# Kernel tuning notes

Hardware: AMD Instinct MI355X
Metric: run time of the kernel (lower is better)

The kernel has to match this reference:

```python
import jax, jax.numpy as jnp
import numpy as np

N, E = 20000, 320000
MEM, IN, HID, H = 128, 256, 128, 2
C = HID               # per-head channels, uniform across layers (see shape constraints)
MSG, TD = 100, 100
ED = MSG + TD         # edge_dim = msg_dim + time_enc.out_channels
L = 3
LN_EPS = 1e-5


def setup_inputs() -> dict:
    key = jax.random.key(0)
    ks = jax.random.split(key, 20)
    f32 = jnp.float32

    def nrm(k, shape, fan):
        return jax.random.normal(k, shape, f32) * (1.0 / np.sqrt(fan)).astype(np.float32)

    return {
        "x": jax.random.normal(ks[0], (N, MEM), f32),
        "last_update": jax.random.uniform(ks[1], (N,), f32) * 1000.0,
        "edge_index": jax.random.randint(ks[2], (2, E), 0, N, jnp.int32),
        "t": jax.random.uniform(ks[3], (E,), f32) * 1000.0,
        "msg": jax.random.normal(ks[4], (E, MSG), f32),
        # TimeEncoder: cos(t * w + b), Linear(1, TD)
        "time_w": nrm(ks[5], (TD,), 1),
        "time_b": nrm(ks[6], (TD,), 1),
        # self.lin: memory_dim -> in_channels
        "lin_w": nrm(ks[7], (MEM, IN), MEM),
        "lin_b": jnp.zeros((IN,), f32),
        # stacked per-layer TransformerConv params (all layers are IN -> H*C = 256)
        "Wq": nrm(ks[8], (L, IN, H * C), IN),
        "bq": jnp.zeros((L, H * C), f32),
        "Wk": nrm(ks[9], (L, IN, H * C), IN),
        "bk": jnp.zeros((L, H * C), f32),
        "Wv": nrm(ks[10], (L, IN, H * C), IN),
        "bv": jnp.zeros((L, H * C), f32),
        "We": nrm(ks[11], (L, ED, H * C), ED),   # lin_edge, bias=False in PyG
        "Wsk": nrm(ks[12], (L, IN, H * C), IN),  # lin_skip (root weight)
        "bsk": jnp.zeros((L, H * C), f32),
        "ln_g": jnp.ones((L, IN), f32),
        "ln_b": jnp.zeros((L, IN), f32),
    }


def _layer_norm(x, g, b):
    mu = jnp.mean(x, axis=-1, keepdims=True)
    var = jnp.mean((x - mu) ** 2, axis=-1, keepdims=True)
    return (x - mu) * jax.lax.rsqrt(var + LN_EPS) * g + b


def _transformer_conv(h, src, dst, eattr, Wq, bq, Wk, bk, Wv, bv, We, Wsk, bsk):
    # h: [N, IN]; eattr: [E, ED]
    q = (h @ Wq + bq).reshape(N, H, C)
    k = (h @ Wk + bk).reshape(N, H, C)
    v = (h @ Wv + bv).reshape(N, H, C)
    e = (eattr @ We).reshape(E, H, C)          # projected edge features
    k_j = k[src] + e                           # [E, H, C]
    alpha = jnp.einsum('ehc,ehc->eh', q[dst], k_j) / np.float32(np.sqrt(C))
    # segment softmax over destination nodes (PyG softmax: exp(a - max)/ (sum + 1e-16))
    amax = jax.ops.segment_max(alpha, dst, num_segments=N)
    ea = jnp.exp(alpha - amax[dst])
    denom = jax.ops.segment_sum(ea, dst, num_segments=N)
    a = ea / (denom[dst] + 1e-16)              # [E, H]
    msg_out = (v[src] + e) * a[:, :, None]     # [E, H, C]
    agg = jax.ops.segment_sum(msg_out, dst, num_segments=N).reshape(N, H * C)
    return agg + h @ Wsk + bsk                 # root/skip connection


def reference(x, last_update, edge_index, t, msg,
              time_w, time_b, lin_w, lin_b,
              Wq, bq, Wk, bk, Wv, bv, We, Wsk, bsk, ln_g, ln_b):
    src, dst = edge_index[0], edge_index[1]
    rel_t = last_update[src] - t                       # [E]
    rel_t_enc = jnp.cos(rel_t[:, None] * time_w + time_b)  # TimeEncoder
    eattr = jnp.concatenate([rel_t_enc, msg], axis=-1)     # [E, ED]
    h = x @ lin_w + lin_b                              # memory_dim != in_channels
    for i in range(L):
        h_new = _transformer_conv(h, src, dst, eattr,
                                  Wq[i], bq[i], Wk[i], bk[i], Wv[i], bv[i],
                                  We[i], Wsk[i], bsk[i])
        h = _layer_norm(h + h_new, ln_g[i], ln_b[i])   # dropout is identity in eval
        if i < L - 1:
            h = jax.nn.silu(h)
    return h
```

## Files before the change

### kernel.cpp

```cpp
#include <hip/hip_runtime.h>
#include <math.h>

constexpr int N_NODES = 20000;
constexpr int N_EDGES = 320000;
constexpr int MEM_D   = 128;
constexpr int IN_D    = 256;
constexpr int HEADS   = 2;
constexpr int CH      = 128;
constexpr int MSG_D   = 100;
constexpr int TD_D    = 100;
constexpr int ED_D    = 200;
constexpr int LAYERS  = 3;

__global__ __launch_bounds__(256) void relt_kernel(
    const int* __restrict__ src, const float* __restrict__ last_update,
    const float* __restrict__ t, float* __restrict__ rel)
{
    int e = blockIdx.x * 256 + threadIdx.x;
    if (e < N_EDGES) rel[e] = last_update[src[e]] - t[e];
}

__global__ __launch_bounds__(256) void time_enc_kernel(
    const float* __restrict__ rel, const float* __restrict__ time_w,
    const float* __restrict__ time_b, float* __restrict__ ct)
{
    __shared__ float sw[TD_D], sb[TD_D];
    int tid = threadIdx.x;
    if (tid < TD_D) { sw[tid] = time_w[tid]; sb[tid] = time_b[tid]; }
    __syncthreads();
    const int total = N_EDGES * TD_D;
    for (int idx = blockIdx.x * 256 + tid; idx < total; idx += gridDim.x * 256) {
        int e = idx / TD_D;
        int d = idx - e * TD_D;
        ct[idx] = cosf(rel[e] * sw[d] + sb[d]);
    }
}

#define BM 64
#define BN 64
#define BK 16
__global__ __launch_bounds__(256) void gemm_f32_kernel(
    const float* __restrict__ A, int lda, long aoff,
    const float* __restrict__ B, int ldb, long boff,
    float* __restrict__ Cm, int ldc, long coff,
    const float* __restrict__ bias,
    int M, int Nn, int K, int accumulate)
{
    A  += (long)blockIdx.z * aoff;
    B  += (long)blockIdx.z * boff;
    Cm += (long)blockIdx.z * coff;

    __shared__ __align__(16) float As[BK][BM + 4];
    __shared__ __align__(16) float Bs[BK][BN + 4];
    int tid = threadIdx.x;
    int tx = tid & 15, ty = tid >> 4;
    int m0 = blockIdx.y * BM, n0 = blockIdx.x * BN;

    float acc[4][4];
#pragma unroll
    for (int i = 0; i < 4; ++i)
#pragma unroll
        for (int j = 0; j < 4; ++j) acc[i][j] = 0.f;

    for (int k0 = 0; k0 < K; k0 += BK) {
#pragma unroll
        for (int i = 0; i < 4; ++i) {
            int li = tid + i * 256;
            int mm = li >> 4, kk = li & 15;
            int gm = m0 + mm, gk = k0 + kk;
            float va = (gm < M && gk < K) ? A[(size_t)gm * lda + gk] : 0.f;
            As[kk][mm] = va;
        }
#pragma unroll
        for (int i = 0; i < 4; ++i) {
            int li = tid + i * 256;
            int kk = li >> 6, nn = li & 63;
            int gk = k0 + kk, gn = n0 + nn;
            float vb = (gk < K && gn < Nn) ? B[(size_t)gk * ldb + gn] : 0.f;
            Bs[kk][nn] = vb;
        }
        __syncthreads();
#pragma unroll
        for (int kk = 0; kk < BK; ++kk) {
            float4 a4 = *(const float4*)&As[kk][ty * 4];
            float4 b4 = *(const float4*)&Bs[kk][tx * 4];
            float av[4] = {a4.x, a4.y, a4.z, a4.w};
            float bv[4] = {b4.x, b4.y, b4.z, b4.w};
#pragma unroll
            for (int i = 0; i < 4; ++i)
#pragma unroll
                for (int j = 0; j < 4; ++j) acc[i][j] += av[i] * bv[j];
        }
        __syncthreads();
    }
#pragma unroll
    for (int i = 0; i < 4; ++i) {
        int gm = m0 + ty * 4 + i;
        if (gm >= M) continue;
#pragma unroll
        for (int j = 0; j < 4; ++j) {
            int gn = n0 + tx * 4 + j;
            if (gn >= Nn) continue;
            float r = acc[i][j];
            if (bias) r += bias[gn];
            size_t off = (size_t)gm * ldc + gn;
            if (accumulate) r += Cm[off];
            Cm[off] = r;
        }
    }
}

#define GBM 128
#define GBN 128
#define GBK 16
__global__ __launch_bounds__(256) void gemm4_f32_kernel(
    const float* __restrict__ A,
    const float* __restrict__ B0, const float* __restrict__ B1,
    const float* __restrict__ B2, const float* __restrict__ B3,
    float* __restrict__ C0, float* __restrict__ C1,
    float* __restrict__ C2, float* __restrict__ C3,
    const float* __restrict__ bias0, const float* __restrict__ bias1,
    const float* __restrict__ bias2, const float* __restrict__ bias3,
    int M)
{
    const float* B; float* C; const float* bias;
    switch (blockIdx.z) {
        case 0: B = B0; C = C0; bias = bias0; break;
        case 1: B = B1; C = C1; bias = bias1; break;
        case 2: B = B2; C = C2; bias = bias2; break;
        default: B = B3; C = C3; bias = bias3; break;
    }
    __shared__ __align__(16) float As[GBK][GBM + 4];
    __shared__ __align__(16) float Bs[GBK][GBN + 4];
    int tid = threadIdx.x;
    int tx = tid & 15, ty = tid >> 4;
    int m0 = blockIdx.y * GBM, n0 = blockIdx.x * GBN;

    float acc00[4][4], acc01[4][4], acc10[4][4], acc11[4][4];
#pragma unroll
    for (int i = 0; i < 4; ++i)
#pragma unroll
        for (int j = 0; j < 4; ++j) {
            acc00[i][j] = 0.f; acc01[i][j] = 0.f;
            acc10[i][j] = 0.f; acc11[i][j] = 0.f;
        }

    for (int k0 = 0; k0 < IN_D; k0 += GBK) {
#pragma unroll
        for (int i = 0; i < 2; ++i) {
            int f = tid + i * 256;
            int row = f >> 2, cb = (f & 3) * 4;
            int gm = m0 + row;
            float4 v;
            if (gm < M) v = *(const float4*)(A + (size_t)gm * IN_D + k0 + cb);
            else { v.x = v.y = v.z = v.w = 0.f; }
            As[cb + 0][row] = v.x;
            As[cb + 1][row] = v.y;
            As[cb + 2][row] = v.z;
            As[cb + 3][row] = v.w;
        }
#pragma unroll
        for (int i = 0; i < 2; ++i) {
            int f = tid + i * 256;
            int kr = f >> 5, cb = (f & 31) * 4;
            float4 v = *(const float4*)(B + (size_t)(k0 + kr) * IN_D + n0 + cb);
            *(float4*)&Bs[kr][cb] = v;
        }
        __syncthreads();
#pragma unroll
        for (int kk = 0; kk < GBK; ++kk) {
            float4 A0 = *(const float4*)&As[kk][ty * 4];
            float4 A1 = *(const float4*)&As[kk][64 + ty * 4];
            float4 Bv0 = *(const float4*)&Bs[kk][tx * 4];
            float4 Bv1 = *(const float4*)&Bs[kk][64 + tx * 4];
            float a0[4] = {A0.x, A0.y, A0.z, A0.w};
            float a1[4] = {A1.x, A1.y, A1.z, A1.w};
            float b0[4] = {Bv0.x, Bv0.y, Bv0.z, Bv0.w};
            float b1[4] = {Bv1.x, Bv1.y, Bv1.z, Bv1.w};
#pragma unroll
            for (int i = 0; i < 4; ++i)
#pragma unroll
                for (int j = 0; j < 4; ++j) {
                    acc00[i][j] += a0[i] * b0[j];
                    acc01[i][j] += a0[i] * b1[j];
                    acc10[i][j] += a1[i] * b0[j];
                    acc11[i][j] += a1[i] * b1[j];
                }
        }
        __syncthreads();
    }
#pragma unroll
    for (int hm = 0; hm < 2; ++hm) {
#pragma unroll
        for (int i = 0; i < 4; ++i) {
            int gm = m0 + hm * 64 + ty * 4 + i;
            if (gm >= M) continue;
            int gn0 = n0 + tx * 4;
            int gn1 = n0 + 64 + tx * 4;
            float4 r0, r1;
            if (hm == 0) {
                r0.x = acc00[i][0]; r0.y = acc00[i][1]; r0.z = acc00[i][2]; r0.w = acc00[i][3];
                r1.x = acc01[i][0]; r1.y = acc01[i][1]; r1.z = acc01[i][2]; r1.w = acc01[i][3];
            } else {
                r0.x = acc10[i][0]; r0.y = acc10[i][1]; r0.z = acc10[i][2]; r0.w = acc10[i][3];
                r1.x = acc11[i][0]; r1.y = acc11[i][1]; r1.z = acc11[i][2]; r1.w = acc11[i][3];
            }
            r0.x += bias[gn0 + 0]; r0.y += bias[gn0 + 1];
            r0.z += bias[gn0 + 2]; r0.w += bias[gn0 + 3];
            r1.x += bias[gn1 + 0]; r1.y += bias[gn1 + 1];
            r1.z += bias[gn1 + 2]; r1.w += bias[gn1 + 3];
            *(float4*)(C + (size_t)gm * IN_D + gn0) = r0;
            *(float4*)(C + (size_t)gm * IN_D + gn1) = r1;
        }
    }
}

__global__ __launch_bounds__(256) void transpose_we_kernel(
    const float* __restrict__ We_l, float* __restrict__ WeT)
{
    int idx = blockIdx.x * 256 + threadIdx.x;
    if (idx >= HEADS * CH * ED_D) return;
    int hh = idx / (CH * ED_D);
    int r = idx - hh * (CH * ED_D);
    int c = r / ED_D;
    int d = r - c * ED_D;
    WeT[idx] = We_l[(size_t)d * IN_D + hh * CH + c];
}

__global__ __launch_bounds__(256) void hist_kernel(const int* __restrict__ dst,
                                                   int* __restrict__ counts)
{
    int e = blockIdx.x * 256 + threadIdx.x;
    if (e < N_EDGES) atomicAdd(&counts[dst[e]], 1);
}

__global__ __launch_bounds__(1024) void scan_kernel(const int* __restrict__ counts,
                                                    int* __restrict__ offsets)
{
    __shared__ int buf[1024];
    __shared__ int carry;
    int tid = threadIdx.x;
    if (tid == 0) carry = 0;
    __syncthreads();
    for (int base = 0; base < N_NODES; base += 1024) {
        int v = (base + tid < N_NODES) ? counts[base + tid] : 0;
        buf[tid] = v;
        __syncthreads();
        for (int off = 1; off < 1024; off <<= 1) {
            int tmp = (tid >= off) ? buf[tid - off] : 0;
            __syncthreads();
            buf[tid] += tmp;
            __syncthreads();
        }
        int incl = buf[tid];
        if (base + tid < N_NODES) offsets[base + tid] = carry + incl - v;
        int blocktot = buf[1023];
        __syncthreads();
        if (tid == 0) carry += blocktot;
        __syncthreads();
    }
    if (tid == 0) offsets[N_NODES] = carry;
}

__global__ __launch_bounds__(256) void copy_int_kernel(const int* __restrict__ a,
                                                       int* __restrict__ b, int n)
{
    int i = blockIdx.x * 256 + threadIdx.x;
    if (i < n) b[i] = a[i];
}

__global__ __launch_bounds__(256) void scatter_kernel(const int* __restrict__ dst,
                                                      int* __restrict__ cursor,
                                                      int* __restrict__ perm)
{
    int e = blockIdx.x * 256 + threadIdx.x;
    if (e < N_EDGES) {
        int p = atomicAdd(&cursor[dst[e]], 1);
        perm[p] = e;
    }
}

__global__ __launch_bounds__(256) void fused_attn_kernel(
    const int* __restrict__ perm, const int* __restrict__ offsets,
    const int* __restrict__ src,
    const float* __restrict__ qmat, const float* __restrict__ kmat,
    const float* __restrict__ vmat, const float* __restrict__ qWe,
    const float* __restrict__ ct, const float* __restrict__ msg,
    float* __restrict__ agg, float* __restrict__ wea)
{
    int n = blockIdx.x;
    int tid = threadIdx.x;
    int start = offsets[n], end = offsets[n + 1];

    __shared__ __align__(16) float sq[IN_D];
    __shared__ float sqw[HEADS * ED_D];
    __shared__ float salpha[64][2];
    __shared__ int   ssrc[64], sedge[64];
    __shared__ float red[256];
    __shared__ float s_m[2], s_s[2], s_r[2];

    sq[tid] = qmat[(size_t)n * IN_D + tid];
    for (int i = tid; i < HEADS * ED_D; i += 256)
        sqw[i] = qWe[(size_t)n * (HEADS * ED_D) + i];
    if (tid < 2) { s_m[tid] = -INFINITY; s_s[tid] = 0.f; }
    __syncthreads();

    float acc = 0.f;
    float wacc_a = 0.f, wacc_b = 0.f;
    const int head_c = tid >> 7;
    const int ha = (tid < ED_D) ? 0 : 1;
    const int da = (tid < ED_D) ? tid : tid - ED_D;
    const int idx2 = tid + 256;
    const int db = idx2 - ED_D;
    const int grp = tid >> 7, lid = tid & 127;
    const int wv = tid >> 6, lane = tid & 63, head = lane >> 5, l = lane & 31;

    for (int base = start; base < end; base += 64) {
        int cnt = min(64, end - base);
        if (tid < cnt) {
            int e = perm[base + tid];
            sedge[tid] = e;
            ssrc[tid] = src[e];
        }
        __syncthreads();

        for (int j = wv; j < cnt; j += 4) {
            int e = sedge[j], s = ssrc[j];
            float4 ka = *(const float4*)(kmat + (size_t)s * IN_D + head * CH + l * 4);
            float4 qa = *(const float4*)(&sq[head * CH + l * 4]);
            float sum = qa.x * ka.x + qa.y * ka.y + qa.z * ka.z + qa.w * ka.w;
            const float* ctrow = ct + (size_t)e * TD_D;
            const float* msgrow = msg + (size_t)e * MSG_D;
            const float* qw = &sqw[head * ED_D];
#pragma unroll
            for (int it = 0; it < 7; ++it) {
                int dd = l + it * 32;
                if (dd < ED_D) {
                    float ev = (dd < TD_D) ? ctrow[dd] : msgrow[dd - TD_D];
                    sum += qw[dd] * ev;
                }
            }
#pragma unroll
            for (int off = 16; off > 0; off >>= 1) sum += __shfl_xor(sum, off, 64);
            if (l == 0) salpha[j][head] = sum * 0.08838834764831845f;
        }
        __syncthreads();

        float pm = -INFINITY;
        for (int j = lid; j < cnt; j += 128) pm = fmaxf(pm, salpha[j][grp]);
        red[tid] = pm;
        __syncthreads();
        for (int s2 = 64; s2 > 0; s2 >>= 1) {
            if (lid < s2) red[tid] = fmaxf(red[tid], red[tid + s2]);
            __syncthreads();
        }
        if (lid == 0) {
            float cm = red[tid];
            float mold = s_m[grp];
            float mnew = fmaxf(mold, cm);
            s_r[grp] = expf(mold - mnew);
            s_m[grp] = mnew;
            s_s[grp] *= s_r[grp];
        }
        __syncthreads();

        float psum = 0.f;
        for (int j = lid; j < cnt; j += 128) {
            float p = expf(salpha[j][grp] - s_m[grp]);
            salpha[j][grp] = p;
            psum += p;
        }
        red[tid] = psum;
        __syncthreads();
        for (int s2 = 64; s2 > 0; s2 >>= 1) {
            if (lid < s2) red[tid] += red[tid + s2];
            __syncthreads();
        }
        if (lid == 0) s_s[grp] += red[tid];

        acc *= s_r[head_c];
        wacc_a *= s_r[ha];
        wacc_b *= s_r[1];
        for (int tt = 0; tt < cnt; ++tt) {
            float p_c = salpha[tt][head_c];
            acc += p_c * vmat[(size_t)ssrc[tt] * IN_D + tid];
            int e = sedge[tt];
            float ev_a = (da < TD_D) ? ct[(size_t)e * TD_D + da]
                                     : msg[(size_t)e * MSG_D + (da - TD_D)];
            wacc_a += salpha[tt][ha] * ev_a;
            if (idx2 < HEADS * ED_D) {
                float ev_b = (db < TD_D) ? ct[(size_t)e * TD_D + db]
                                         : msg[(size_t)e * MSG_D + (db - TD_D)];
                wacc_b += salpha[tt][1] * ev_b;
            }
        }
        __syncthreads();
    }

    float inv_c = 1.f / (s_s[head_c] + 1e-16f);
    agg[(size_t)n * IN_D + tid] = acc * inv_c;
    float inv_a = 1.f / (s_s[ha] + 1e-16f);
    wea[(size_t)n * (HEADS * ED_D) + tid] = wacc_a * inv_a;
    if (idx2 < HEADS * ED_D) {
        float inv_b = 1.f / (s_s[1] + 1e-16f);
        wea[(size_t)n * (HEADS * ED_D) + idx2] = wacc_b * inv_b;
    }
}

__global__ __launch_bounds__(256) void ln_kernel(
    const float* __restrict__ hprev, const float* __restrict__ agg,
    const float* __restrict__ hskip,
    const float* __restrict__ g, const float* __restrict__ b,
    float* __restrict__ out, int do_silu)
{
    int n = blockIdx.x, c = threadIdx.x;
    size_t off = (size_t)n * IN_D + c;
    float y = hprev[off] + agg[off] + hskip[off];
    __shared__ float red[256];
    red[c] = y;
    __syncthreads();
    for (int s = 128; s > 0; s >>= 1) {
        if (c < s) red[c] += red[c + s];
        __syncthreads();
    }
    float mu = red[0] * (1.f / 256.f);
    __syncthreads();
    float dy = y - mu;
    red[c] = dy * dy;
    __syncthreads();
    for (int s = 128; s > 0; s >>= 1) {
        if (c < s) red[c] += red[c + s];
        __syncthreads();
    }
    float var = red[0] * (1.f / 256.f);
    float r = dy * (1.f / sqrtf(var + 1e-5f)) * g[c] + b[c];
    if (do_silu) r = r / (1.f + expf(-r));
    out[off] = r;
}

extern "C" void kernel_launch(void* const* d_in, const int* in_sizes, int n_in,
                              void* d_out, int out_size, void* d_ws, size_t ws_size,
                              hipStream_t stream)
{
    const float* x           = (const float*)d_in[0];
    const float* last_update = (const float*)d_in[1];
    const int*   edge_index  = (const int*)d_in[2];
    const float* t           = (const float*)d_in[3];
    const float* msg         = (const float*)d_in[4];
    const float* time_w      = (const float*)d_in[5];
    const float* time_b      = (const float*)d_in[6];
    const float* lin_w       = (const float*)d_in[7];
    const float* lin_b       = (const float*)d_in[8];
    const float* Wq          = (const float*)d_in[9];
    const float* bq          = (const float*)d_in[10];
    const float* Wk          = (const float*)d_in[11];
    const float* bk          = (const float*)d_in[12];
    const float* Wv          = (const float*)d_in[13];
    const float* bv          = (const float*)d_in[14];
    const float* We          = (const float*)d_in[15];
    const float* Wsk         = (const float*)d_in[16];
    const float* bsk         = (const float*)d_in[17];
    const float* ln_g        = (const float*)d_in[18];
    const float* ln_b        = (const float*)d_in[19];

    const int* srcIdx = edge_index;
    const int* dstIdx = edge_index + N_EDGES;

    float* fw = (float*)d_ws;
    float* ct    = fw; fw += (size_t)N_EDGES * TD_D;
    float* relb  = fw; fw += (size_t)N_EDGES;
    float* h     = fw; fw += (size_t)N_NODES * IN_D;
    float* h2    = fw; fw += (size_t)N_NODES * IN_D;
    float* qbuf  = fw; fw += (size_t)N_NODES * IN_D;
    float* kbuf  = fw; fw += (size_t)N_NODES * IN_D;
    float* vbuf  = fw; fw += (size_t)N_NODES * IN_D;
    float* hskip = fw; fw += (size_t)N_NODES * IN_D;
    float* aggb  = fw; fw += (size_t)N_NODES * IN_D;
    float* qWeb  = fw; fw += (size_t)N_NODES * HEADS * ED_D;
    float* weab  = fw; fw += (size_t)N_NODES * HEADS * ED_D;
    float* WeT   = fw; fw += (size_t)HEADS * CH * ED_D;
    int* iw = (int*)fw;
    int* counts  = iw; iw += N_NODES;
    int* offsets = iw; iw += N_NODES + 1;
    int* cursor  = iw; iw += N_NODES;
    int* perm    = iw; iw += N_EDGES;

    auto gemmz = [&](const float* A, int lda, long aoff,
                     const float* B, int ldb, long boff,
                     float* C, int ldc, long coff,
                     const float* bias, int M, int Nn, int K, int acc, int nz) {
        dim3 grid((Nn + BN - 1) / BN, (M + BM - 1) / BM, nz);
        gemm_f32_kernel<<<grid, 256, 0, stream>>>(A, lda, aoff, B, ldb, boff,
                                                  C, ldc, coff, bias, M, Nn, K, acc);
    };

    relt_kernel<<<(N_EDGES + 255) / 256, 256, 0, stream>>>(srcIdx, last_update, t, relb);
    time_enc_kernel<<<2048, 256, 0, stream>>>(relb, time_w, time_b, ct);

    gemmz(x, MEM_D, 0, lin_w, IN_D, 0, h, IN_D, 0, lin_b, N_NODES, IN_D, MEM_D, 0, 1);

    hipMemsetAsync(counts, 0, N_NODES * sizeof(int), stream);
    hist_kernel<<<(N_EDGES + 255) / 256, 256, 0, stream>>>(dstIdx, counts);
    scan_kernel<<<1, 1024, 0, stream>>>(counts, offsets);
    copy_int_kernel<<<(N_NODES + 255) / 256, 256, 0, stream>>>(offsets, cursor, N_NODES);
    scatter_kernel<<<(N_EDGES + 255) / 256, 256, 0, stream>>>(dstIdx, cursor, perm);

    float* bufs[2] = {h, h2};
    for (int layer = 0; layer < LAYERS; ++layer) {
        const float* Wq_l  = Wq  + (size_t)layer * IN_D * IN_D;
        const float* Wk_l  = Wk  + (size_t)layer * IN_D * IN_D;
        const float* Wv_l  = Wv  + (size_t)layer * IN_D * IN_D;
        const float* Wsk_l = Wsk + (size_t)layer * IN_D * IN_D;
        const float* We_l  = We  + (size_t)layer * ED_D * IN_D;
        const float* bq_l  = bq  + (size_t)layer * IN_D;
        const float* bk_l  = bk  + (size_t)layer * IN_D;
        const float* bv_l  = bv  + (size_t)layer * IN_D;
        const float* bsk_l = bsk + (size_t)layer * IN_D;

        float* hin  = bufs[layer & 1];
        float* hout = (layer == LAYERS - 1) ? (float*)d_out : bufs[(layer + 1) & 1];

        {
            dim3 grid(IN_D / GBN, (N_NODES + GBM - 1) / GBM, 4);
            gemm4_f32_kernel<<<grid, 256, 0, stream>>>(
                hin, Wq_l, Wk_l, Wv_l, Wsk_l,
                qbuf, kbuf, vbuf, hskip,
                bq_l, bk_l, bv_l, bsk_l, N_NODES);
        }

        transpose_we_kernel<<<(HEADS * CH * ED_D + 255) / 256, 256, 0, stream>>>(We_l, WeT);
        gemmz(qbuf, IN_D, CH, WeT, ED_D, (long)CH * ED_D,
              qWeb, HEADS * ED_D, ED_D, nullptr, N_NODES, ED_D, CH, 0, HEADS);

        fused_attn_kernel<<<N_NODES, 256, 0, stream>>>(
            perm, offsets, srcIdx, qbuf, kbuf, vbuf, qWeb, ct, msg, aggb, weab);

        gemmz(weab, HEADS * ED_D, ED_D, We_l, IN_D, CH,
              aggb, IN_D, CH, nullptr, N_NODES, CH, ED_D, 1, HEADS);

        ln_kernel<<<N_NODES, 256, 0, stream>>>(
            hin, aggb, hskip, ln_g + (size_t)layer * IN_D, ln_b + (size_t)layer * IN_D,
            hout, layer < LAYERS - 1 ? 1 : 0);
    }
}
```

Measured before the change: 1.918 ms.

## Drop online-max softmax reductions and stage edge features in shared memory

The fused attention kernel no longer keeps a running max with rescaling. Each score is exponentiated directly, the denominator is summed in registers per wave, and a single small reduction happens at the end, which removes several block-wide tree reductions and barriers per chunk. Edge features read during the score pass are now cached in a shared tile, so the aggregation loop reads LDS instead of gathering ct/msg from global memory again. The chunk size drops from 64 to 32 so the tile fits. The cost is that exp without max subtraction can overflow if attention logits are large.

```diff
diff --git a/kernel.cpp b/kernel.cpp
--- a/kernel.cpp
+++ b/kernel.cpp
@@ -11,6 +11,7 @@
 constexpr int TD_D    = 100;
 constexpr int ED_D    = 200;
 constexpr int LAYERS  = 3;
+constexpr int CHK     = 32;
 
 __global__ __launch_bounds__(256) void relt_kernel(
     const int* __restrict__ src, const float* __restrict__ last_update,
@@ -294,29 +295,28 @@
 
     __shared__ __align__(16) float sq[IN_D];
     __shared__ float sqw[HEADS * ED_D];
-    __shared__ float salpha[64][2];
-    __shared__ int   ssrc[64], sedge[64];
-    __shared__ float red[256];
-    __shared__ float s_m[2], s_s[2], s_r[2];
+    __shared__ float se[CHK][ED_D];
+    __shared__ float sp[CHK][2];
+    __shared__ int   ssrc[CHK], sedge[CHK];
+    __shared__ float spart[8];
 
     sq[tid] = qmat[(size_t)n * IN_D + tid];
     for (int i = tid; i < HEADS * ED_D; i += 256)
         sqw[i] = qWe[(size_t)n * (HEADS * ED_D) + i];
-    if (tid < 2) { s_m[tid] = -INFINITY; s_s[tid] = 0.f; }
-    __syncthreads();
-
-    float acc = 0.f;
-    float wacc_a = 0.f, wacc_b = 0.f;
+    __syncthreads();
+
+    const int wv = tid >> 6, lane = tid & 63, head = lane >> 5, l = lane & 31;
     const int head_c = tid >> 7;
     const int ha = (tid < ED_D) ? 0 : 1;
     const int da = (tid < ED_D) ? tid : tid - ED_D;
     const int idx2 = tid + 256;
     const int db = idx2 - ED_D;
-    const int grp = tid >> 7, lid = tid & 127;
-    const int wv = tid >> 6, lane = tid & 63, head = lane >> 5, l = lane & 31;
-
-    for (int base = start; base < end; base += 64) {
-        int cnt = min(64, end - base);
+
+    float psum_reg = 0.f;
+    float acc = 0.f, wacc_a = 0.f, wacc_b = 0.f;
+
+    for (int base = start; base < end; base += CHK) {
+        int cnt = min(CHK, end - base);
         if (tid < cnt) {
             int e = perm[base + tid];
             sedge[tid] = e;
@@ -337,74 +337,39 @@
                 int dd = l + it * 32;
                 if (dd < ED_D) {
                     float ev = (dd < TD_D) ? ctrow[dd] : msgrow[dd - TD_D];
+                    if (head == 0) se[j][dd] = ev;
                     sum += qw[dd] * ev;
                 }
             }
 #pragma unroll
             for (int off = 16; off > 0; off >>= 1) sum += __shfl_xor(sum, off, 64);
-            if (l == 0) salpha[j][head] = sum * 0.08838834764831845f;
-        }
-        __syncthreads();
-
-        float pm = -INFINITY;
-        for (int j = lid; j < cnt; j += 128) pm = fmaxf(pm, salpha[j][grp]);
-        red[tid] = pm;
-        __syncthreads();
-        for (int s2 = 64; s2 > 0; s2 >>= 1) {
-            if (lid < s2) red[tid] = fmaxf(red[tid], red[tid + s2]);
-            __syncthreads();
-        }
-        if (lid == 0) {
-            float cm = red[tid];
-            float mold = s_m[grp];
-            float mnew = fmaxf(mold, cm);
-            s_r[grp] = expf(mold - mnew);
-            s_m[grp] = mnew;
-            s_s[grp] *= s_r[grp];
-        }
-        __syncthreads();
-
-        float psum = 0.f;
-        for (int j = lid; j < cnt; j += 128) {
-            float p = expf(salpha[j][grp] - s_m[grp]);
-            salpha[j][grp] = p;
-            psum += p;
-        }
-        red[tid] = psum;
-        __syncthreads();
-        for (int s2 = 64; s2 > 0; s2 >>= 1) {
-            if (lid < s2) red[tid] += red[tid + s2];
-            __syncthreads();
-        }
-        if (lid == 0) s_s[grp] += red[tid];
-
-        acc *= s_r[head_c];
-        wacc_a *= s_r[ha];
-        wacc_b *= s_r[1];
+            float p = expf(sum * 0.08838834764831845f);
+            if (l == 0) { sp[j][head] = p; psum_reg += p; }
+        }
+        __syncthreads();
+
+#pragma unroll 4
         for (int tt = 0; tt < cnt; ++tt) {
-            float p_c = salpha[tt][head_c];
-            acc += p_c * vmat[(size_t)ssrc[tt] * IN_D + tid];
-            int e = sedge[tt];
-            float ev_a = (da < TD_D) ? ct[(size_t)e * TD_D + da]
-                                     : msg[(size_t)e * MSG_D + (da - TD_D)];
-            wacc_a += salpha[tt][ha] * ev_a;
-            if (idx2 < HEADS * ED_D) {
-                float ev_b = (db < TD_D) ? ct[(size_t)e * TD_D + db]
-                                         : msg[(size_t)e * MSG_D + (db - TD_D)];
-                wacc_b += salpha[tt][1] * ev_b;
-            }
-        }
-        __syncthreads();
-    }
-
-    float inv_c = 1.f / (s_s[head_c] + 1e-16f);
-    agg[(size_t)n * IN_D + tid] = acc * inv_c;
-    float inv_a = 1.f / (s_s[ha] + 1e-16f);
-    wea[(size_t)n * (HEADS * ED_D) + tid] = wacc_a * inv_a;
-    if (idx2 < HEADS * ED_D) {
-        float inv_b = 1.f / (s_s[1] + 1e-16f);
-        wea[(size_t)n * (HEADS * ED_D) + idx2] = wacc_b * inv_b;
-    }
+            float p0 = sp[tt][0], p1 = sp[tt][1];
+            acc += (head_c ? p1 : p0) * vmat[(size_t)ssrc[tt] * IN_D + tid];
+            wacc_a += (ha ? p1 : p0) * se[tt][da];
+            if (tid < 144) wacc_b += p1 * se[tt][db];
+        }
+        __syncthreads();
+    }
+
+    if (l == 0) spart[wv * 2 + head] = psum_reg;
+    __syncthreads();
+    if (tid < 2) {
+        float s = spart[tid] + spart[2 + tid] + spart[4 + tid] + spart[6 + tid];
+        spart[tid] = 1.f / (s + 1e-16f);
+    }
+    __syncthreads();
+
+    agg[(size_t)n * IN_D + tid] = acc * spart[head_c];
+    wea[(size_t)n * (HEADS * ED_D) + tid] = wacc_a * spart[ha];
+    if (tid < 144)
+        wea[(size_t)n * (HEADS * ED_D) + idx2] = wacc_b * spart[1];
 }
 
 __global__ __launch_bounds__(256) void ln_kernel(
```

Result: slower. 2.239 ms (+16.7%).
